# Optimization experiments

Measured on AMD Instinct MI355X. Metric: run time of the kernel, lower is better.

## Reference

```python
import jax, jax.numpy as jnp
import numpy as np
from jax import lax

B, T1, T2, C = 8, 128, 128, 256
K = 3

def setup_inputs() -> dict:
    key = jax.random.key(0)
    k1, k2, kw, kb = jax.random.split(key, 4)
    x1 = jax.random.normal(k1, (B, T1, C), dtype=jnp.float32)
    x2 = jax.random.normal(k2, (B, T2, C), dtype=jnp.float32)
    # conv2d: in_channels = 2C, out_channels = C, kernel 3x3 (OIHW)
    fan_in = 2 * C * K * K
    bound = 1.0 / np.sqrt(fan_in)
    W = jax.random.uniform(kw, (C, 2 * C, K, K), jnp.float32, -bound, bound)
    b = jax.random.uniform(kb, (C,), jnp.float32, -bound, bound)
    alpha = jnp.float32(0.5)
    return {"x1": x1, "x2": x2, "W": W, "b": b, "alpha": alpha}


def reference(x1, x2, W, b, alpha):
    # x1: [B, T1, C], x2: [B, T2, C]
    a = jnp.transpose(x1, (0, 2, 1))  # [B, C, T1]
    c2 = jnp.transpose(x2, (0, 2, 1))  # [B, C, T2]
    Bd, Cd, T1d = a.shape
    T2d = c2.shape[-1]
    # joint outer-product tensor: [B, 2C, T1, T2]
    j1 = jnp.broadcast_to(a[:, :, :, None], (Bd, Cd, T1d, T2d))
    j2 = jnp.broadcast_to(c2[:, :, None, :], (Bd, Cd, T1d, T2d))
    joint = jnp.concatenate([j1, j2], axis=1)
    out = lax.conv_general_dilated(
        joint, W, window_strides=(1, 1), padding="SAME",
        dimension_numbers=("NCHW", "OIHW", "NCHW"))
    out = out + b[None, :, None, None]
    out = jax.nn.gelu(out, approximate=False)  # torch nn.GELU default = exact erf
    out_T1 = jnp.mean(out, axis=-1)            # [B, C, T1]
    out_T1 = jnp.transpose(out_T1, (0, 2, 1))  # [B, T1, C]
    return out_T1 * alpha + x1
```

## Files before the change

kernel.cpp:

```cpp
#include <hip/hip_runtime.h>
#include <math.h>

#define B_   8
#define T_   128
#define C_   256
#define XLDS 264
#define WLDP 136

typedef unsigned short ushort;
typedef ushort ushort8v __attribute__((ext_vector_type(8)));
typedef __bf16 bf16x8  __attribute__((ext_vector_type(8)));
typedef float  f32x4   __attribute__((ext_vector_type(4)));

__device__ __forceinline__ ushort f2bf(float f) {
    unsigned u = __float_as_uint(f);
    u += 0x7fffu + ((u >> 16) & 1u);
    return (ushort)(u >> 16);
}

__device__ __forceinline__ float gelu_fast(float x) {
    float x2 = x * x;
    float y2 = x * fmaf(-0.10294234f, x2, -2.30220818f);
    float e  = __builtin_amdgcn_exp2f(y2);
    return x * __builtin_amdgcn_rcpf(1.0f + e);
}

__device__ __forceinline__ ushort8v pack8(float4 lo, float4 hi) {
    ushort8v u;
    u[0] = f2bf(lo.x); u[1] = f2bf(lo.y); u[2] = f2bf(lo.z); u[3] = f2bf(lo.w);
    u[4] = f2bf(hi.x); u[5] = f2bf(hi.y); u[6] = f2bf(hi.z); u[7] = f2bf(hi.w);
    return u;
}

__global__ __launch_bounds__(256) void tc_packw(
    const float* __restrict__ W, ushort* __restrict__ Wt)
{
    const int o = blockIdx.x, t = threadIdx.x;
    __shared__ ushort lw[4608];
    const float* src = W + (size_t)o * 4608;
    #pragma unroll
    for (int i = 0; i < 18; ++i)
        lw[t + i * 256] = f2bf(src[t + i * 256]);
    __syncthreads();
    #pragma unroll
    for (int i = 0; i < 18; ++i) {
        int d  = t + i * 256;
        int s  = d / 2304;
        int e  = d - s * 2304;
        int nj = e / 768;
        int k  = e - nj * 768;
        int sh = k >> 8, ci = k & 255;
        ushort v = (s == 0) ? lw[ci * 9 + sh * 3 + nj]
                            : lw[(256 + ci) * 9 + nj * 3 + sh];
        Wt[((size_t)s * 768 + o * 3 + nj) * 768 + k] = v;
    }
}

__global__ __launch_bounds__(256, 4) void tc_gemm(
    const float* __restrict__ x1, const float* __restrict__ x2,
    const ushort* __restrict__ Wt, float* __restrict__ AB)
{
    __shared__ ushort Xs[34 * XLDS];
    __shared__ ushort Ws[64 * WLDP];

    const int tn = blockIdx.x;
    const int tm = blockIdx.y;
    const int s  = blockIdx.z;
    const int u  = threadIdx.x;
    const int l  = u & 63, w = u >> 6;
    const int wr = w >> 1, wc = w & 1;
    const int r16 = l & 15, kb = l >> 4;

    const int b_     = tm >> 2;
    const int t_base = (tm & 3) * 32;
    const float*  Xb = (s ? x2 : x1) + (size_t)b_ * T_ * C_;
    const ushort* Wb = Wt + ((size_t)s * 768 + tn * 64) * 768;

    {
        #pragma unroll
        for (int j = 0; j < 5; ++j) {
            int c = u + j * 256;
            if (j < 4 || c < 1088) {
                int i  = c >> 5;
                int kc = (c & 31) * 8;
                int t  = t_base + i - 1;
                ushort8v v = {};
                if (t >= 0 && t < T_) {
                    const float* p = Xb + (size_t)t * C_ + kc;
                    v = pack8(*(const float4*)p, *(const float4*)(p + 4));
                }
                *(ushort8v*)&Xs[i * XLDS + kc] = v;
            }
        }
    }

    ushort8v wbuf[4];
    #pragma unroll
    for (int j = 0; j < 4; ++j) {
        int c = u + j * 256;
        wbuf[j] = *(const ushort8v*)(Wb + (size_t)(c >> 4) * 768 + (c & 15) * 8);
    }

    f32x4 acc[2] = {};
    #pragma unroll
    for (int r = 0; r < 6; ++r) {
        const int sh = r >> 1, p = r & 1;
        __syncthreads();
        #pragma unroll
        for (int j = 0; j < 4; ++j) {
            int c = u + j * 256;
            *(ushort8v*)&Ws[(c >> 4) * WLDP + (c & 15) * 8] = wbuf[j];
        }
        if (r < 5) {
            const int rn = r + 1;
            const ushort* wsrc = Wb + (rn >> 1) * 256 + (rn & 1) * 128;
            #pragma unroll
            for (int j = 0; j < 4; ++j) {
                int c = u + j * 256;
                wbuf[j] = *(const ushort8v*)(wsrc + (size_t)(c >> 4) * 768 + (c & 15) * 8);
            }
        }
        __syncthreads();
        #pragma unroll
        for (int ks = 0; ks < 4; ++ks) {
            const int ka  = p * 128 + ks * 32 + kb * 8;
            const int kw_ = ks * 32 + kb * 8;
            bf16x8 a0 = __builtin_bit_cast(bf16x8,
                *(const ushort8v*)&Xs[(wr * 16 + r16 + sh) * XLDS + ka]);
            bf16x8 b0 = __builtin_bit_cast(bf16x8,
                *(const ushort8v*)&Ws[(wc * 32 + r16) * WLDP + kw_]);
            bf16x8 b1 = __builtin_bit_cast(bf16x8,
                *(const ushort8v*)&Ws[(wc * 32 + 16 + r16) * WLDP + kw_]);
            acc[0] = __builtin_amdgcn_mfma_f32_16x16x32_bf16(a0, b0, acc[0], 0, 0, 0);
            acc[1] = __builtin_amdgcn_mfma_f32_16x16x32_bf16(a0, b1, acc[1], 0, 0, 0);
        }
    }

    #pragma unroll
    for (int j = 0; j < 2; ++j) {
        int n = tn * 64 + wc * 32 + j * 16 + r16;
        int m = tm * 32 + wr * 16 + kb * 4;
        *(f32x4*)&AB[((size_t)s * 768 + n) * 1024 + m] = acc[j];
    }
}

__global__ __launch_bounds__(128) void tc_fin(
    const float* __restrict__ AB, const float* __restrict__ x1,
    const float* __restrict__ bias, const float* __restrict__ alpha_p,
    float* __restrict__ out)
{
    const int o = blockIdx.x & 255;
    const int b = blockIdx.x >> 8;
    const int t = threadIdx.x;

    __shared__ float Bv[3][T_];

    const float* A0 = AB + ((size_t)o * 3) * 1024 + b * T_ + t;
    const float* A1 = AB + ((size_t)768 + o * 3) * 1024 + b * T_ + t;
    float a0 = A0[0], a1 = A0[1024], a2 = A0[2048];
    float b0 = A1[0], b1 = A1[1024], b2 = A1[2048];

    const float bo = bias[o];
    float A3 = bo + a0 + a1 + a2;
    float Al = bo + a1 + a2;
    float Ar = bo + a0 + a1;
    Bv[0][t] = b0 + b1 + b2;
    Bv[1][t] = b1 + b2;
    Bv[2][t] = b0 + b1;
    __syncthreads();

    int cls = (t == 0) ? 1 : ((t == T_ - 1) ? 2 : 0);
    const float* Bs = Bv[cls];
    float s0 = 0.f, s1 = 0.f, s2 = 0.f, s3 = 0.f;
    for (int j = 0; j < T_; j += 4) {
        f32x4 v = *(const f32x4*)&Bs[j];
        s0 += gelu_fast(A3 + v[0]); s1 += gelu_fast(A3 + v[1]);
        s2 += gelu_fast(A3 + v[2]); s3 += gelu_fast(A3 + v[3]);
    }
    float sm = (s0 + s1) + (s2 + s3);
    float bl = Bs[0], br = Bs[T_ - 1];
    sm += gelu_fast(Al + bl) - gelu_fast(A3 + bl);
    sm += gelu_fast(Ar + br) - gelu_fast(A3 + br);

    const float kk2 = (*alpha_p) * (1.0f / (float)T_);
    size_t go = ((size_t)(b * T_ + t)) * C_ + o;
    out[go] = sm * kk2 + x1[go];
}

extern "C" void kernel_launch(void* const* d_in, const int* in_sizes, int n_in,
                              void* d_out, int out_size, void* d_ws, size_t ws_size,
                              hipStream_t stream) {
    const float* x1    = (const float*)d_in[0];
    const float* x2    = (const float*)d_in[1];
    const float* W     = (const float*)d_in[2];
    const float* bias  = (const float*)d_in[3];
    const float* alpha = (const float*)d_in[4];
    float* out = (float*)d_out;

    float*  AB = (float*)d_ws;
    ushort* Wt = (ushort*)((char*)d_ws + (size_t)2 * 768 * 1024 * 4);

    tc_packw<<<256, 256, 0, stream>>>(W, Wt);
    tc_gemm<<<dim3(12, 32, 2), 256, 0, stream>>>(x1, x2, Wt, AB);
    tc_fin<<<B_ * C_, T_, 0, stream>>>(AB, x1, bias, alpha, out);
}
```

Baseline: 91.03 us.

## Double GEMM M-tile per block and pack two outputs per finisher block

The GEMM block tile grows from 32 to 64 rows of time, so each wave computes a 2x2 set of MFMA tiles and reuses the B fragments across two A fragments. This halves the grid and the redundant weight staging per output row, at the cost of more LDS and registers (occupancy hint lowered to 3). The finisher kernel now handles two (b,o) pairs per 256-thread block to cut block count and launch overhead. The larger tile leaves fewer blocks (384) to spread across the GPU's compute units.

```diff
diff --git a/kernel.cpp b/kernel.cpp
--- a/kernel.cpp
+++ b/kernel.cpp
@@ -56,11 +56,11 @@
     }
 }
 
-__global__ __launch_bounds__(256, 4) void tc_gemm(
+__global__ __launch_bounds__(256, 3) void tc_gemm(
     const float* __restrict__ x1, const float* __restrict__ x2,
     const ushort* __restrict__ Wt, float* __restrict__ AB)
 {
-    __shared__ ushort Xs[34 * XLDS];
+    __shared__ ushort Xs[66 * XLDS];
     __shared__ ushort Ws[64 * WLDP];
 
     const int tn = blockIdx.x;
@@ -71,16 +71,16 @@
     const int wr = w >> 1, wc = w & 1;
     const int r16 = l & 15, kb = l >> 4;
 
-    const int b_     = tm >> 2;
-    const int t_base = (tm & 3) * 32;
+    const int b_     = tm >> 1;
+    const int t_base = (tm & 1) * 64;
     const float*  Xb = (s ? x2 : x1) + (size_t)b_ * T_ * C_;
     const ushort* Wb = Wt + ((size_t)s * 768 + tn * 64) * 768;
 
     {
         #pragma unroll
-        for (int j = 0; j < 5; ++j) {
+        for (int j = 0; j < 9; ++j) {
             int c = u + j * 256;
-            if (j < 4 || c < 1088) {
+            if (j < 8 || c < 2112) {
                 int i  = c >> 5;
                 int kc = (c & 31) * 8;
                 int t  = t_base + i - 1;
@@ -101,7 +101,7 @@
         wbuf[j] = *(const ushort8v*)(Wb + (size_t)(c >> 4) * 768 + (c & 15) * 8);
     }
 
-    f32x4 acc[2] = {};
+    f32x4 acc[2][2] = {};
     #pragma unroll
     for (int r = 0; r < 6; ++r) {
         const int sh = r >> 1, p = r & 1;
@@ -126,34 +126,43 @@
             const int ka  = p * 128 + ks * 32 + kb * 8;
             const int kw_ = ks * 32 + kb * 8;
             bf16x8 a0 = __builtin_bit_cast(bf16x8,
-                *(const ushort8v*)&Xs[(wr * 16 + r16 + sh) * XLDS + ka]);
+                *(const ushort8v*)&Xs[(wr * 32 + r16 + sh) * XLDS + ka]);
+            bf16x8 a1 = __builtin_bit_cast(bf16x8,
+                *(const ushort8v*)&Xs[(wr * 32 + 16 + r16 + sh) * XLDS + ka]);
             bf16x8 b0 = __builtin_bit_cast(bf16x8,
                 *(const ushort8v*)&Ws[(wc * 32 + r16) * WLDP + kw_]);
             bf16x8 b1 = __builtin_bit_cast(bf16x8,
                 *(const ushort8v*)&Ws[(wc * 32 + 16 + r16) * WLDP + kw_]);
-            acc[0] = __builtin_amdgcn_mfma_f32_16x16x32_bf16(a0, b0, acc[0], 0, 0, 0);
-            acc[1] = __builtin_amdgcn_mfma_f32_16x16x32_bf16(a0, b1, acc[1], 0, 0, 0);
+            acc[0][0] = __builtin_amdgcn_mfma_f32_16x16x32_bf16(a0, b0, acc[0][0], 0, 0, 0);
+            acc[0][1] = __builtin_amdgcn_mfma_f32_16x16x32_bf16(a0, b1, acc[0][1], 0, 0, 0);
+            acc[1][0] = __builtin_amdgcn_mfma_f32_16x16x32_bf16(a1, b0, acc[1][0], 0, 0, 0);
+            acc[1][1] = __builtin_amdgcn_mfma_f32_16x16x32_bf16(a1, b1, acc[1][1], 0, 0, 0);
         }
     }
 
     #pragma unroll
     for (int j = 0; j < 2; ++j) {
         int n = tn * 64 + wc * 32 + j * 16 + r16;
-        int m = tm * 32 + wr * 16 + kb * 4;
-        *(f32x4*)&AB[((size_t)s * 768 + n) * 1024 + m] = acc[j];
-    }
-}
-
-__global__ __launch_bounds__(128) void tc_fin(
+        #pragma unroll
+        for (int i = 0; i < 2; ++i) {
+            int m = tm * 64 + wr * 32 + i * 16 + kb * 4;
+            *(f32x4*)&AB[((size_t)s * 768 + n) * 1024 + m] = acc[i][j];
+        }
+    }
+}
+
+__global__ __launch_bounds__(256) void tc_fin(
     const float* __restrict__ AB, const float* __restrict__ x1,
     const float* __restrict__ bias, const float* __restrict__ alpha_p,
     float* __restrict__ out)
 {
-    const int o = blockIdx.x & 255;
-    const int b = blockIdx.x >> 8;
-    const int t = threadIdx.x;
-
-    __shared__ float Bv[3][T_];
+    const int p   = threadIdx.x >> 7;
+    const int t   = threadIdx.x & 127;
+    const int idx = blockIdx.x * 2 + p;
+    const int o   = idx & 255;
+    const int b   = idx >> 8;
+
+    __shared__ float Bv[2][3][T_];
 
     const float* A0 = AB + ((size_t)o * 3) * 1024 + b * T_ + t;
     const float* A1 = AB + ((size_t)768 + o * 3) * 1024 + b * T_ + t;
@@ -164,13 +173,13 @@
     float A3 = bo + a0 + a1 + a2;
     float Al = bo + a1 + a2;
     float Ar = bo + a0 + a1;
-    Bv[0][t] = b0 + b1 + b2;
-    Bv[1][t] = b1 + b2;
-    Bv[2][t] = b0 + b1;
+    Bv[p][0][t] = b0 + b1 + b2;
+    Bv[p][1][t] = b1 + b2;
+    Bv[p][2][t] = b0 + b1;
     __syncthreads();
 
     int cls = (t == 0) ? 1 : ((t == T_ - 1) ? 2 : 0);
-    const float* Bs = Bv[cls];
+    const float* Bs = Bv[p][cls];
     float s0 = 0.f, s1 = 0.f, s2 = 0.f, s3 = 0.f;
     for (int j = 0; j < T_; j += 4) {
         f32x4 v = *(const f32x4*)&Bs[j];
@@ -201,6 +210,6 @@
     ushort* Wt = (ushort*)((char*)d_ws + (size_t)2 * 768 * 1024 * 4);
 
     tc_packw<<<256, 256, 0, stream>>>(W, Wt);
-    tc_gemm<<<dim3(12, 32, 2), 256, 0, stream>>>(x1, x2, Wt, AB);
-    tc_fin<<<B_ * C_, T_, 0, stream>>>(AB, x1, bias, alpha, out);
-}
+    tc_gemm<<<dim3(12, 16, 2), 256, 0, stream>>>(x1, x2, Wt, AB);
+    tc_fin<<<B_ * C_ / 2, 256, 0, stream>>>(AB, x1, bias, alpha, out);
+}
```

Measured after the change: 90.74 us. About the same (-0.3%).
